# Kernel optimization log

Measured on AMD Instinct MI355X. Metric: run time of the kernel, lower is better.

The kernel has to match this reference:

```python
import jax, jax.numpy as jnp
import numpy as np

N, E, G = 20000, 320000, 64
IN_DIM, EDGE_DIM, H, L = 23, 6, 256, 4
NEG = 0.2   # leaky_relu negative slope (GATv2 default)
EPS = 1e-5  # layernorm eps


def setup_inputs() -> dict:
    key = jax.random.key(0)
    ks = jax.random.split(key, 12)
    g = lambda k, shape: jax.random.normal(k, shape, jnp.float32) * 0.05
    return {
        "x": jax.random.normal(ks[0], (N, IN_DIM), jnp.float32),
        "edge_index": jax.random.randint(ks[1], (2, E), 0, N),
        "edge_attr": jax.random.uniform(ks[2], (E, EDGE_DIM), dtype=jnp.float32),
        "batch": jnp.sort(jax.random.randint(ks[3], (N,), 0, G)),
        "W_l0": g(ks[4], (IN_DIM, H)),
        "W_r0": g(ks[5], (IN_DIM, H)),
        "W_l": g(ks[6], (L - 1, H, H)),
        "W_r": g(ks[7], (L - 1, H, H)),
        "b_l": jnp.zeros((L, H), jnp.float32),
        "b_r": jnp.zeros((L, H), jnp.float32),
        "W_e": g(ks[8], (L, EDGE_DIM, H)),
        "att": g(ks[9], (L, H)),
        "bias": jnp.zeros((L, H), jnp.float32),
        "ln_w": jnp.ones((L, H), jnp.float32),
        "ln_b": jnp.zeros((L, H), jnp.float32),
        "lin_W": g(ks[10], (H, H)),
        "lin_b": jnp.zeros((H,), jnp.float32),
    }


def _segment_softmax(logits, seg, n):
    m = jax.ops.segment_max(logits, seg, num_segments=n)  # every node has a self loop -> finite
    e = jnp.exp(logits - m[seg])
    s = jax.ops.segment_sum(e, seg, num_segments=n)
    return e / s[seg]


def _gatv2(h, src, dst, e_emb, Wl, bl, Wr, br, a, bout):
    n = h.shape[0]
    hl = h @ Wl + bl  # source transform [N, H]
    hr = h @ Wr + br  # target transform [N, H]
    m = hl[src] + hr[dst] + e_emb              # [E', H]
    m = jnp.where(m > 0, m, NEG * m)           # leaky_relu
    alpha = _segment_softmax(m @ a, dst, n)    # [E']
    out = jax.ops.segment_sum(hl[src] * alpha[:, None], dst, num_segments=n)
    return out + bout


def _layernorm(x, w, b):
    mu = x.mean(-1, keepdims=True)
    var = ((x - mu) ** 2).mean(-1, keepdims=True)
    return (x - mu) * jax.lax.rsqrt(var + EPS) * w + b


def reference(x, edge_index, edge_attr, batch, W_l0, W_r0, W_l, W_r, b_l, b_r,
              W_e, att, bias, ln_w, ln_b, lin_W, lin_b):
    n = x.shape[0]
    src, dst = edge_index[0], edge_index[1]
    # add self loops; self-loop edge_attr = mean of incoming edge_attr (fill_value='mean')
    ones_e = jnp.ones((src.shape[0],), x.dtype)
    deg = jax.ops.segment_sum(ones_e, dst, num_segments=n)
    loop_attr = jax.ops.segment_sum(edge_attr, dst, num_segments=n) / jnp.maximum(deg, 1.0)[:, None]
    loops = jnp.arange(n, dtype=src.dtype)
    src_f = jnp.concatenate([src, loops])
    dst_f = jnp.concatenate([dst, loops])
    ea = jnp.concatenate([edge_attr, loop_attr], axis=0)  # [E+N, 6]

    Wls = [W_l0] + [W_l[i] for i in range(L - 1)]
    Wrs = [W_r0] + [W_r[i] for i in range(L - 1)]
    h = x
    for i in range(L):
        e_emb = ea @ W_e[i]  # [E+N, H]
        h = _gatv2(h, src_f, dst_f, e_emb, Wls[i], b_l[i], Wrs[i], b_r[i], att[i], bias[i])
        h = _layernorm(h, ln_w[i], ln_b[i])
        h = jax.nn.relu(h)
    h = h @ lin_W + lin_b  # final jk='last' projection
    # global mean pool over graphs
    cnt = jax.ops.segment_sum(jnp.ones((n,), h.dtype), batch, num_segments=G)
    pooled = jax.ops.segment_sum(h, batch, num_segments=G) / jnp.maximum(cnt, 1.0)[:, None]
    return pooled
```

## Files before the change

### kernel.cpp

```cpp
#include <hip/hip_runtime.h>
#include <hip/hip_bf16.h>
#include <math.h>

#define H 256
#define EDIM 6
#define NEG 0.2f
#define LN_EPS 1e-5f
#define NPAD 20096

typedef __bf16 bf16x8 __attribute__((ext_vector_type(8)));
typedef float  floatx4 __attribute__((ext_vector_type(4)));
typedef float  f32x2   __attribute__((ext_vector_type(2)));

__device__ __forceinline__ float b2f(unsigned short u) {
    union { unsigned int i; float f; } v; v.i = ((unsigned int)u) << 16; return v.f;
}
__device__ __forceinline__ unsigned short f2bu(float f) {
    __hip_bfloat16 h = __float2bfloat16(f);
    return *(unsigned short*)&h;
}

__global__ void k_edge_hist(const int* __restrict__ ei, int* __restrict__ deg, int E) {
    int e = blockIdx.x * blockDim.x + threadIdx.x;
    if (e >= E) return;
    atomicAdd(&deg[ei[E + e]], 1);
}

__global__ __launch_bounds__(256) void k_scan1(const int* __restrict__ deg,
                                               int* __restrict__ row_ptr,
                                               int* __restrict__ bsum, int N) {
    __shared__ int ws[4];
    int tid = threadIdx.x, gid = blockIdx.x * 256 + tid;
    int lane = tid & 63, w = tid >> 6;
    int v = (gid < N) ? deg[gid] : 0;
    int x = v;
#pragma unroll
    for (int d = 1; d < 64; d <<= 1) { int y = __shfl_up(x, d); if (lane >= d) x += y; }
    if (lane == 63) ws[w] = x;
    __syncthreads();
    int off = 0;
#pragma unroll
    for (int i = 0; i < 4; i++) off += (i < w) ? ws[i] : 0;
    if (gid < N) row_ptr[gid] = off + x - v;
    if (tid == 255) bsum[blockIdx.x] = off + x;
}

__global__ __launch_bounds__(256) void k_scan2(int* __restrict__ bsum, int nb) {
    __shared__ int ws[4];
    int tid = threadIdx.x;
    int lane = tid & 63, w = tid >> 6;
    int v = (tid < nb) ? bsum[tid] : 0;
    int x = v;
#pragma unroll
    for (int d = 1; d < 64; d <<= 1) { int y = __shfl_up(x, d); if (lane >= d) x += y; }
    if (lane == 63) ws[w] = x;
    __syncthreads();
    int off = 0;
#pragma unroll
    for (int i = 0; i < 4; i++) off += (i < w) ? ws[i] : 0;
    if (tid < nb) bsum[tid] = off + x - v;
}

__global__ __launch_bounds__(256) void k_scan3(int* __restrict__ row_ptr,
                                               int* __restrict__ cursor,
                                               const int* __restrict__ bsum, int N, int E) {
    int gid = blockIdx.x * 256 + threadIdx.x;
    if (gid < N) {
        int v = row_ptr[gid] + bsum[blockIdx.x];
        row_ptr[gid] = v;
        cursor[gid] = v;
    }
    if (gid == 0) row_ptr[N] = E;
}

__global__ void k_scatter(const int* __restrict__ ei, const float* __restrict__ eattr,
                          int* __restrict__ cursor, float4* __restrict__ erec, int E) {
    int e = blockIdx.x * blockDim.x + threadIdx.x;
    if (e >= E) return;
    int s = ei[e], d = ei[E + e];
    int pos = atomicAdd(&cursor[d], 1);
    float4 ra, rb;
    ra.x = __int_as_float(s << 10);
    ra.y = eattr[e * EDIM + 0];
    ra.z = eattr[e * EDIM + 1];
    ra.w = eattr[e * EDIM + 2];
    rb.x = eattr[e * EDIM + 3];
    rb.y = eattr[e * EDIM + 4];
    rb.z = eattr[e * EDIM + 5];
    rb.w = 0.f;
    erec[(size_t)pos * 2]     = ra;
    erec[(size_t)pos * 2 + 1] = rb;
}

__global__ __launch_bounds__(256) void k_loop_mean(const int* __restrict__ row_ptr,
                                                   const float4* __restrict__ erec,
                                                   float* __restrict__ loop_attr, int N) {
    int wv = threadIdx.x >> 6, lane = threadIdx.x & 63;
    int node = blockIdx.x * 4 + wv;
    if (node >= N) return;
    int e0 = row_ptr[node], e1 = row_ptr[node + 1];
    float es[6] = {0.f, 0.f, 0.f, 0.f, 0.f, 0.f};
    for (int e = e0 + lane; e < e1; e += 64) {
        float4 ra = erec[(size_t)e * 2];
        float4 rb = erec[(size_t)e * 2 + 1];
        es[0] += ra.y; es[1] += ra.z; es[2] += ra.w;
        es[3] += rb.x; es[4] += rb.y; es[5] += rb.z;
    }
#pragma unroll
    for (int d = 1; d < 64; d <<= 1) {
#pragma unroll
        for (int k = 0; k < 6; k++) es[k] += __shfl_xor(es[k], d);
    }
    if (lane == 0) {
        float inv = 1.f / fmaxf((float)(e1 - e0), 1.f);
        float4 a, b;
        a.x = es[0] * inv; a.y = es[1] * inv; a.z = es[2] * inv; a.w = es[3] * inv;
        b.x = es[4] * inv; b.y = es[5] * inv; b.z = 0.f; b.w = 0.f;
        *(float4*)&loop_attr[(size_t)node * 8]     = a;
        *(float4*)&loop_attr[(size_t)node * 8 + 4] = b;
    }
}

__global__ __launch_bounds__(256) void k_conv_all(
    const float* __restrict__ x, const float* __restrict__ Wl0,
    const float* __restrict__ Wr0, const float* __restrict__ Wl,
    const float* __restrict__ Wr,
    __hip_bfloat16* __restrict__ xb, __hip_bfloat16* __restrict__ w0t,
    __hip_bfloat16* __restrict__ wbig, int N) {
    int idx = blockIdx.x * 256 + threadIdx.x;
    const int XN = NPAD * 32;
    if (idx < XN) {
        int r = idx >> 5, k = idx & 31;
        float v = (r < N && k < 23) ? x[r * 23 + k] : 0.f;
        xb[idx] = __float2bfloat16(v);
        return;
    }
    idx -= XN;
    if (idx < 16384) {
        int mat = idx >> 13, rem = idx & 8191;
        int c = rem >> 5, k = rem & 31;
        const float* W = mat ? Wr0 : Wl0;
        float v = (k < 23) ? W[k * 256 + c] : 0.f;
        w0t[idx] = __float2bfloat16(v);
        return;
    }
    idx -= 16384;
    if (idx < 6 * 65536) {
        int mat = idx >> 16, rem = idx & 65535;
        int c = rem >> 8, k = rem & 255;
        const float* W = (mat < 3) ? (Wl + (size_t)mat * 65536)
                       : (Wr + (size_t)(mat - 3) * 65536);
        wbig[idx] = __float2bfloat16(W[k * 256 + c]);
    }
}

template<int K>
__global__ __launch_bounds__(256) void k_gemm_mfma(
    const __hip_bfloat16* __restrict__ A, int N,
    const __hip_bfloat16* __restrict__ Wt1, const float* __restrict__ b1,
    float* __restrict__ C1,
    const __hip_bfloat16* __restrict__ Wt2, const float* __restrict__ b2,
    float* __restrict__ C2) {
    int tid = threadIdx.x;
    int wv = tid >> 6, lane = tid & 63;
    int quad = lane >> 4, l16 = lane & 15;
    int mat = blockIdx.x >> 1;
    int c0 = (blockIdx.x & 1) * 128;
    int r0 = blockIdx.y * 128;
    const __hip_bfloat16* Wt = mat ? Wt2 : Wt1;
    const float* bv = mat ? b2 : b1;
    float* C = mat ? C2 : C1;
    int wm = wv >> 1, wn = wv & 1;
    int rbase = r0 + wm * 64;
    int cbase = c0 + wn * 64;

    floatx4 acc[4][4] = {};
    const __bf16* Ab = (const __bf16*)A;
    const __bf16* Bb = (const __bf16*)Wt;

    if constexpr (K == 32) {
        bf16x8 a[4], b[4];
        const __bf16* Ap = Ab + (size_t)(rbase + l16) * K + quad * 8;
#pragma unroll
        for (int mi = 0; mi < 4; mi++)
            a[mi] = *(const bf16x8*)(Ap + (size_t)mi * 16 * K);
        const __bf16* Bp = Bb + (size_t)(cbase + l16) * K + quad * 8;
#pragma unroll
        for (int ni = 0; ni < 4; ni++)
            b[ni] = *(const bf16x8*)(Bp + (size_t)ni * 16 * K);
#pragma unroll
        for (int mi = 0; mi < 4; mi++)
#pragma unroll
            for (int ni = 0; ni < 4; ni++)
                acc[mi][ni] = __builtin_amdgcn_mfma_f32_16x16x32_bf16(a[mi], b[ni], acc[mi][ni], 0, 0, 0);
    } else {
        __shared__ __align__(16) __bf16 As[128 * 32];
        __shared__ __align__(16) __bf16 Bs[128 * 32];
        int srow = wv * 16 + (lane >> 2);
        int sseg = lane & 3;
        for (int k0 = 0; k0 < K; k0 += 32) {
#pragma unroll
            for (int j = 0; j < 2; j++) {
                int row = j * 64 + srow;
                const __bf16* gA = Ab + (size_t)(r0 + row) * K + k0 + sseg * 8;
                __builtin_amdgcn_global_load_lds(
                    (const __attribute__((address_space(1))) void*)gA,
                    (__attribute__((address_space(3))) void*)(As + j * 2048 + wv * 512),
                    16, 0, 0);
                const __bf16* gB = Bb + (size_t)(c0 + row) * K + k0 + sseg * 8;
                __builtin_amdgcn_global_load_lds(
                    (const __attribute__((address_space(1))) void*)gB,
                    (__attribute__((address_space(3))) void*)(Bs + j * 2048 + wv * 512),
                    16, 0, 0);
            }
            __syncthreads();
            bf16x8 a[4], b[4];
#pragma unroll
            for (int mi = 0; mi < 4; mi++)
                a[mi] = *(const bf16x8*)(As + (wm * 64 + mi * 16 + l16) * 32 + quad * 8);
#pragma unroll
            for (int ni = 0; ni < 4; ni++)
                b[ni] = *(const bf16x8*)(Bs + (wn * 64 + ni * 16 + l16) * 32 + quad * 8);
#pragma unroll
            for (int mi = 0; mi < 4; mi++)
#pragma unroll
                for (int ni = 0; ni < 4; ni++)
                    acc[mi][ni] = __builtin_amdgcn_mfma_f32_16x16x32_bf16(a[mi], b[ni], acc[mi][ni], 0, 0, 0);
            __syncthreads();
        }
    }
#pragma unroll
    for (int ni = 0; ni < 4; ni++) {
        int c = cbase + ni * 16 + l16;
        float bb = bv[c];
#pragma unroll
        for (int mi = 0; mi < 4; mi++) {
#pragma unroll
            for (int r = 0; r < 4; r++) {
                int gr = rbase + mi * 16 + quad * 4 + r;
                if (gr < N) C[(size_t)gr * H + c] = acc[mi][ni][r] + bb;
            }
        }
    }
}

__global__ __launch_bounds__(64) void k_gat(
    const float* __restrict__ hlf, const float* __restrict__ hr,
    const int* __restrict__ row_ptr, const float4* __restrict__ erec,
    const float* __restrict__ loop_attr,
    const float* __restrict__ We, const float* __restrict__ attv,
    const float* __restrict__ bias, const float* __restrict__ lnw,
    const float* __restrict__ lnb, unsigned short* __restrict__ hout, int N) {
    int lane = threadIdx.x & 63;
    int node = blockIdx.x;
    if (node >= N) return;
    int cb = lane * 4;
    int cb4 = cb * 4;
    const char* hbase = (const char*)hlf;
    bool b0 = (lane & 1) != 0;
    bool b1 = (lane & 2) != 0;

    f32x2 we2[EDIM][2];
#pragma unroll
    for (int k = 0; k < EDIM; k++) {
        float4 t = *(const float4*)&We[k * H + cb];
        we2[k][0] = (f32x2){t.x, t.y};
        we2[k][1] = (f32x2){t.z, t.w};
    }
    float4 t;
    t = *(const float4*)&attv[cb];
    f32x2 av0 = {t.x, t.y}, av1 = {t.z, t.w};
    t = *(const float4*)&hr[(size_t)node * H + cb];
    f32x2 hr0 = {t.x, t.y}, hr1 = {t.z, t.w};
    t = *(const float4*)&hlf[(size_t)node * H + cb];
    f32x2 hl0 = {t.x, t.y}, hl1 = {t.z, t.w};

    float denom = 0.f;
    f32x2 acc0 = {0.f, 0.f}, acc1 = {0.f, 0.f};

    int e0 = row_ptr[node], e1 = row_ptr[node + 1];
    int deg = e1 - e0;
    int gfull = deg >> 2;

    for (int g = 0; g <= gfull; g++) {
        int trem = (g == gfull) ? (deg & 3) : 4;
        if (trem == 0) break;
        int base = e0 + g * 4;
        f32x2 hsa[4], hsb[4];
        float p[4];
#pragma unroll
        for (int i = 0; i < 4; i++) {
            int idx = (i < trem) ? (base + i) : base;
            float4 ra = erec[(size_t)idx * 2];
            float4 rb = erec[(size_t)idx * 2 + 1];
            float4 h4 = *(const float4*)(hbase + (__float_as_int(ra.x) + cb4));
            hsa[i] = (f32x2){h4.x, h4.y};
            hsb[i] = (f32x2){h4.z, h4.w};
            f32x2 t0 = hr0, t1 = hr1;
            t0 += ra.y * we2[0][0]; t1 += ra.y * we2[0][1];
            t0 += ra.z * we2[1][0]; t1 += ra.z * we2[1][1];
            t0 += ra.w * we2[2][0]; t1 += ra.w * we2[2][1];
            t0 += rb.x * we2[3][0]; t1 += rb.x * we2[3][1];
            t0 += rb.y * we2[4][0]; t1 += rb.y * we2[4][1];
            t0 += rb.z * we2[5][0]; t1 += rb.z * we2[5][1];
            f32x2 v0 = hsa[i] + t0;
            f32x2 v1 = hsb[i] + t1;
            v0 = __builtin_elementwise_max(v0, v0 * NEG);
            v1 = __builtin_elementwise_max(v1, v1 * NEG);
            f32x2 pd = v0 * av0;
            pd += v1 * av1;
            p[i] = pd.x + pd.y;
        }
        float a01 = b0 ? p[1] : p[0];
        float c01 = b0 ? p[0] : p[1];
        a01 += __shfl_xor(c01, 1);
        float a23 = b0 ? p[3] : p[2];
        float c23 = b0 ? p[2] : p[3];
        a23 += __shfl_xor(c23, 1);
        float u = b1 ? a23 : a01;
        float v = b1 ? a01 : a23;
        u += __shfl_xor(v, 2);
        u += __shfl_xor(u, 4);
        u += __shfl_xor(u, 8);
        u += __shfl_xor(u, 16);
        u += __shfl_xor(u, 32);
        float w = ((lane & 3) < trem) ? __expf(u) : 0.f;
        float wx1 = __shfl_xor(w, 1);
        float wx2 = __shfl_xor(w, 2);
        float wx3 = __shfl_xor(wx1, 2);
        denom += (w + wx1) + (wx2 + wx3);
        float x0 = b0 ? wx1 : w,   x1 = b0 ? w   : wx1;
        float x2 = b0 ? wx3 : wx2, x3 = b0 ? wx2 : wx3;
        float w0 = b1 ? x2 : x0, w1 = b1 ? x3 : x1;
        float w2 = b1 ? x0 : x2, w3 = b1 ? x1 : x3;
        acc0 += w0 * hsa[0]; acc1 += w0 * hsb[0];
        acc0 += w1 * hsa[1]; acc1 += w1 * hsb[1];
        acc0 += w2 * hsa[2]; acc1 += w2 * hsb[2];
        acc0 += w3 * hsa[3]; acc1 += w3 * hsb[3];
    }

    {
        float4 la0 = *(const float4*)&loop_attr[(size_t)node * 8];
        float4 la1 = *(const float4*)&loop_attr[(size_t)node * 8 + 4];
        f32x2 t0 = hl0 + hr0, t1 = hl1 + hr1;
        t0 += la0.x * we2[0][0]; t1 += la0.x * we2[0][1];
        t0 += la0.y * we2[1][0]; t1 += la0.y * we2[1][1];
        t0 += la0.z * we2[2][0]; t1 += la0.z * we2[2][1];
        t0 += la0.w * we2[3][0]; t1 += la0.w * we2[3][1];
        t0 += la1.x * we2[4][0]; t1 += la1.x * we2[4][1];
        t0 += la1.y * we2[5][0]; t1 += la1.y * we2[5][1];
        t0 = __builtin_elementwise_max(t0, t0 * NEG);
        t1 = __builtin_elementwise_max(t1, t1 * NEG);
        f32x2 pd = t0 * av0;
        pd += t1 * av1;
        float p = pd.x + pd.y;
#pragma unroll
        for (int d = 1; d < 64; d <<= 1) p += __shfl_xor(p, d);
        float w = __expf(p);
        denom += w;
        acc0 += w * hl0; acc1 += w * hl1;
    }

    float inv = 1.f / denom;
    t = *(const float4*)&bias[cb];
    float o0 = acc0.x * inv + t.x;
    float o1 = acc0.y * inv + t.y;
    float o2 = acc1.x * inv + t.z;
    float o3 = acc1.y * inv + t.w;

    float s = (o0 + o1) + (o2 + o3);
    float q = fmaf(o0, o0, fmaf(o1, o1, fmaf(o2, o2, o3 * o3)));
    float a = b0 ? q : s;
    float c = b0 ? s : q;
    a += __shfl_xor(c, 1);
    a += __shfl_xor(a, 2);
    a += __shfl_xor(a, 4);
    a += __shfl_xor(a, 8);
    a += __shfl_xor(a, 16);
    a += __shfl_xor(a, 32);
    float other = __shfl_xor(a, 1);
    float stot = b0 ? other : a;
    float qtot = b0 ? a : other;
    float mu = stot * (1.f / 256.f);
    float var = fmaf(-mu, mu, qtot * (1.f / 256.f));
    float rstd = rsqrtf(fmaxf(var, 0.f) + LN_EPS);

    float4 w4 = *(const float4*)&lnw[cb];
    float4 b4 = *(const float4*)&lnb[cb];
    ushort4 outv;
    outv.x = f2bu(fmaxf((o0 - mu) * rstd * w4.x + b4.x, 0.f));
    outv.y = f2bu(fmaxf((o1 - mu) * rstd * w4.y + b4.y, 0.f));
    outv.z = f2bu(fmaxf((o2 - mu) * rstd * w4.z + b4.z, 0.f));
    outv.w = f2bu(fmaxf((o3 - mu) * rstd * w4.w + b4.w, 0.f));
    *(ushort4*)&hout[(size_t)node * H + cb] = outv;
}

__global__ __launch_bounds__(256) void k_pool_sum(
    const unsigned short* __restrict__ hb, const int* __restrict__ batch,
    float* __restrict__ pooled, int N) {
    int c = threadIdx.x;
    int chunk = (N + gridDim.x - 1) / gridDim.x;
    int n0 = blockIdx.x * chunk;
    int n1 = min(n0 + chunk, N);
    if (n0 >= n1) return;
    float acc = 0.f;
    int cur = batch[n0];
    for (int n = n0; n < n1; n++) {
        int g = batch[n];
        if (g != cur) {
            atomicAdd(&pooled[cur * H + c], acc);
            acc = 0.f; cur = g;
        }
        acc += b2f(hb[(size_t)n * H + c]);
    }
    atomicAdd(&pooled[cur * H + c], acc);
}

__global__ __launch_bounds__(256) void k_lin_pool(
    const float* __restrict__ pooled, const int* __restrict__ batch,
    const float* __restrict__ linW, const float* __restrict__ linb,
    float* __restrict__ out, int N) {
    __shared__ float row[H];
    __shared__ int s_lo, s_hi;
    int g = blockIdx.x, c = threadIdx.x;
    if (c == 0) {
        int lo = 0, hi = N;
        while (lo < hi) { int mid = (lo + hi) >> 1; if (batch[mid] < g) lo = mid + 1; else hi = mid; }
        s_lo = lo;
    }
    if (c == 1) {
        int lo = 0, hi = N;
        while (lo < hi) { int mid = (lo + hi) >> 1; if (batch[mid] < g + 1) lo = mid + 1; else hi = mid; }
        s_hi = lo;
    }
    __syncthreads();
    int cnt = s_hi - s_lo;
    float scale = (cnt > 0) ? 1.f / (float)cnt : 0.f;
    row[c] = pooled[g * H + c] * scale;
    __syncthreads();
    float acc = (cnt > 0) ? linb[c] : 0.f;
#pragma unroll 8
    for (int k = 0; k < H; k++) acc = fmaf(row[k], linW[k * H + c], acc);
    out[g * H + c] = acc;
}

extern "C" void kernel_launch(void* const* d_in, const int* in_sizes, int n_in,
                              void* d_out, int out_size, void* d_ws, size_t ws_size,
                              hipStream_t stream) {
    const float* x        = (const float*)d_in[0];
    const int*   ei       = (const int*)d_in[1];
    const float* eattr    = (const float*)d_in[2];
    const int*   batch    = (const int*)d_in[3];
    const float* W_l0     = (const float*)d_in[4];
    const float* W_r0     = (const float*)d_in[5];
    const float* W_l      = (const float*)d_in[6];
    const float* W_r      = (const float*)d_in[7];
    const float* b_l      = (const float*)d_in[8];
    const float* b_r      = (const float*)d_in[9];
    const float* W_e      = (const float*)d_in[10];
    const float* att      = (const float*)d_in[11];
    const float* bias     = (const float*)d_in[12];
    const float* ln_w     = (const float*)d_in[13];
    const float* ln_b     = (const float*)d_in[14];
    const float* lin_W    = (const float*)d_in[15];
    const float* lin_b    = (const float*)d_in[16];

    const int N = in_sizes[0] / 23;
    const int E = in_sizes[1] / 2;
    const int G = out_size / H;
    const int L = 4;

    char* p = (char*)d_ws;
    float* hlf = (float*)p;                       p += (size_t)N * H * 4;
    float* hr  = (float*)p;                       p += (size_t)N * H * 4;
    float4* erec = (float4*)p;                    p += (size_t)E * 32;
    unsigned short* hb = (unsigned short*)p;      p += (size_t)NPAD * H * 2;
    __hip_bfloat16* xb  = (__hip_bfloat16*)p;     p += (size_t)NPAD * 32 * 2;
    __hip_bfloat16* w0t = (__hip_bfloat16*)p;     p += (size_t)2 * 256 * 32 * 2;
    __hip_bfloat16* wbig = (__hip_bfloat16*)p;    p += (size_t)6 * 65536 * 2;
    float* loop_attr = (float*)p;                 p += (size_t)N * 8 * 4;
    float* pooled = (float*)p;                    p += (size_t)G * H * 4;
    int* deg      = (int*)p;                      p += (size_t)N * 4;
    int* row_ptr  = (int*)p;                      p += (size_t)(N + 1) * 4;
    int* cursor   = (int*)p;                      p += (size_t)N * 4;
    int* bsum     = (int*)p;                      p += (size_t)256 * 4;

    __hip_bfloat16* Wl0t = w0t;
    __hip_bfloat16* Wr0t = w0t + 8192;
    __hip_bfloat16* Wlt  = wbig;
    __hip_bfloat16* Wrt  = wbig + (size_t)3 * 65536;

    hipMemsetAsync(deg, 0, (size_t)N * sizeof(int), stream);
    hipMemsetAsync(pooled, 0, (size_t)G * H * sizeof(float), stream);
    hipMemsetAsync(hb + (size_t)N * H, 0, (size_t)(NPAD - N) * H * 2, stream);

    int tb = 256;
    int conv_total = NPAD * 32 + 16384 + 6 * 65536;
    k_conv_all<<<(conv_total + tb - 1) / tb, tb, 0, stream>>>(x, W_l0, W_r0, W_l, W_r,
                                                              xb, w0t, wbig, N);

    k_edge_hist<<<(E + tb - 1) / tb, tb, 0, stream>>>(ei, deg, E);
    int nb = (N + 255) / 256;
    k_scan1<<<nb, 256, 0, stream>>>(deg, row_ptr, bsum, N);
    k_scan2<<<1, 256, 0, stream>>>(bsum, nb);
    k_scan3<<<nb, 256, 0, stream>>>(row_ptr, cursor, bsum, N, E);
    k_scatter<<<(E + tb - 1) / tb, tb, 0, stream>>>(ei, eattr, cursor, erec, E);
    k_loop_mean<<<(N + 3) / 4, 256, 0, stream>>>(row_ptr, erec, loop_attr, N);

    dim3 gdual(4, NPAD / 128), blk(256);

    for (int l = 0; l < L; l++) {
        const __hip_bfloat16* A  = (l == 0) ? xb : (const __hip_bfloat16*)hb;
        const __hip_bfloat16* Wl = (l == 0) ? Wl0t : (Wlt + (size_t)(l - 1) * 65536);
        const __hip_bfloat16* Wr = (l == 0) ? Wr0t : (Wrt + (size_t)(l - 1) * 65536);
        if (l == 0)
            k_gemm_mfma<32><<<gdual, blk, 0, stream>>>(A, N, Wl, b_l + l * H, hlf,
                                                       Wr, b_r + l * H, hr);
        else
            k_gemm_mfma<256><<<gdual, blk, 0, stream>>>(A, N, Wl, b_l + l * H, hlf,
                                                        Wr, b_r + l * H, hr);
        k_gat<<<N, 64, 0, stream>>>(hlf, hr, row_ptr, erec, loop_attr,
                                    W_e + (size_t)l * EDIM * H, att + l * H,
                                    bias + l * H, ln_w + l * H, ln_b + l * H, hb, N);
    }

    k_pool_sum<<<256, 256, 0, stream>>>(hb, batch, pooled, N);
    k_lin_pool<<<G, 256, 0, stream>>>(pooled, batch, lin_W, lin_b, (float*)d_out, N);
}
```

Measured before the change: 460.0 us.

## Preload full weight slice into LDS once and fold memsets into conversion kernel

The K=256 GEMM path now loads the block's whole 128x256 weight slice into padded shared memory once, then reads A fragments directly from global memory each k-step. This drops the per-k-step LDS staging of both A and B and the two barriers per iteration. Separately, the three hipMemsetAsync calls are folded into the existing conversion kernel to cut launch overhead. In exchange, shared-memory use grows to about 66 KB per block, which may reduce occupancy, and A reads become uncoalesced strided global loads.

```diff
diff --git a/kernel.cpp b/kernel.cpp
--- a/kernel.cpp
+++ b/kernel.cpp
@@ -7,6 +7,7 @@
 #define NEG 0.2f
 #define LN_EPS 1e-5f
 #define NPAD 20096
+#define BSTRIDE 260
 
 typedef __bf16 bf16x8 __attribute__((ext_vector_type(8)));
 typedef float  floatx4 __attribute__((ext_vector_type(4)));
@@ -126,7 +127,8 @@
     const float* __restrict__ Wr0, const float* __restrict__ Wl,
     const float* __restrict__ Wr,
     __hip_bfloat16* __restrict__ xb, __hip_bfloat16* __restrict__ w0t,
-    __hip_bfloat16* __restrict__ wbig, int N) {
+    __hip_bfloat16* __restrict__ wbig, int* __restrict__ deg,
+    float* __restrict__ pooled, unsigned int* __restrict__ hbpad, int N) {
     int idx = blockIdx.x * 256 + threadIdx.x;
     const int XN = NPAD * 32;
     if (idx < XN) {
@@ -151,7 +153,14 @@
         const float* W = (mat < 3) ? (Wl + (size_t)mat * 65536)
                        : (Wr + (size_t)(mat - 3) * 65536);
         wbig[idx] = __float2bfloat16(W[k * 256 + c]);
-    }
+        return;
+    }
+    idx -= 6 * 65536;
+    if (idx < N) { deg[idx] = 0; return; }
+    idx -= N;
+    if (idx < 16384) { pooled[idx] = 0.f; return; }
+    idx -= 16384;
+    if (idx < (NPAD - 20000) * 128) hbpad[idx] = 0u;
 }
 
 template<int K>
@@ -194,39 +203,31 @@
             for (int ni = 0; ni < 4; ni++)
                 acc[mi][ni] = __builtin_amdgcn_mfma_f32_16x16x32_bf16(a[mi], b[ni], acc[mi][ni], 0, 0, 0);
     } else {
-        __shared__ __align__(16) __bf16 As[128 * 32];
-        __shared__ __align__(16) __bf16 Bs[128 * 32];
-        int srow = wv * 16 + (lane >> 2);
-        int sseg = lane & 3;
+        __shared__ __align__(16) __bf16 Bs[128 * BSTRIDE];
+#pragma unroll
+        for (int i = 0; i < 16; i++) {
+            int seg = tid + i * 256;
+            int col = seg >> 5;
+            int off = (seg & 31) * 8;
+            bf16x8 v = *(const bf16x8*)(Bb + (size_t)(c0 + col) * 256 + off);
+            *(bf16x8*)&Bs[col * BSTRIDE + off] = v;
+        }
+        __syncthreads();
+#pragma unroll 4
         for (int k0 = 0; k0 < K; k0 += 32) {
-#pragma unroll
-            for (int j = 0; j < 2; j++) {
-                int row = j * 64 + srow;
-                const __bf16* gA = Ab + (size_t)(r0 + row) * K + k0 + sseg * 8;
-                __builtin_amdgcn_global_load_lds(
-                    (const __attribute__((address_space(1))) void*)gA,
-                    (__attribute__((address_space(3))) void*)(As + j * 2048 + wv * 512),
-                    16, 0, 0);
-                const __bf16* gB = Bb + (size_t)(c0 + row) * K + k0 + sseg * 8;
-                __builtin_amdgcn_global_load_lds(
-                    (const __attribute__((address_space(1))) void*)gB,
-                    (__attribute__((address_space(3))) void*)(Bs + j * 2048 + wv * 512),
-                    16, 0, 0);
-            }
-            __syncthreads();
             bf16x8 a[4], b[4];
+            const __bf16* Ap = Ab + (size_t)(rbase + l16) * K + k0 + quad * 8;
 #pragma unroll
             for (int mi = 0; mi < 4; mi++)
-                a[mi] = *(const bf16x8*)(As + (wm * 64 + mi * 16 + l16) * 32 + quad * 8);
+                a[mi] = *(const bf16x8*)(Ap + (size_t)mi * 16 * K);
 #pragma unroll
             for (int ni = 0; ni < 4; ni++)
-                b[ni] = *(const bf16x8*)(Bs + (wn * 64 + ni * 16 + l16) * 32 + quad * 8);
+                b[ni] = *(const bf16x8*)&Bs[(wn * 64 + ni * 16 + l16) * BSTRIDE + k0 + quad * 8];
 #pragma unroll
             for (int mi = 0; mi < 4; mi++)
 #pragma unroll
                 for (int ni = 0; ni < 4; ni++)
                     acc[mi][ni] = __builtin_amdgcn_mfma_f32_16x16x32_bf16(a[mi], b[ni], acc[mi][ni], 0, 0, 0);
-            __syncthreads();
         }
     }
 #pragma unroll
@@ -490,14 +491,11 @@
     __hip_bfloat16* Wlt  = wbig;
     __hip_bfloat16* Wrt  = wbig + (size_t)3 * 65536;
 
-    hipMemsetAsync(deg, 0, (size_t)N * sizeof(int), stream);
-    hipMemsetAsync(pooled, 0, (size_t)G * H * sizeof(float), stream);
-    hipMemsetAsync(hb + (size_t)N * H, 0, (size_t)(NPAD - N) * H * 2, stream);
-
     int tb = 256;
-    int conv_total = NPAD * 32 + 16384 + 6 * 65536;
-    k_conv_all<<<(conv_total + tb - 1) / tb, tb, 0, stream>>>(x, W_l0, W_r0, W_l, W_r,
-                                                              xb, w0t, wbig, N);
+    int conv_total = NPAD * 32 + 16384 + 6 * 65536 + N + 16384 + (NPAD - N) * 128;
+    k_conv_all<<<(conv_total + tb - 1) / tb, tb, 0, stream>>>(
+        x, W_l0, W_r0, W_l, W_r, xb, w0t, wbig, deg, pooled,
+        (unsigned int*)(hb + (size_t)N * H), N);
 
     k_edge_hist<<<(E + tb - 1) / tb, tb, 0, stream>>>(ei, deg, E);
     int nb = (N + 255) / 256;
```

New measurement: 495.3 us. 7.7% more time.

## Store source-transform features in bf16 and fold memsets into conversion kernel

Applied to the files above, without the earlier changes.

The source-side transform hl is now written by the GEMM as bf16 instead of fp32, and the GAT kernel gathers it as ushort4 and widens it to float. This halves the bytes of the random per-edge gather and also halves the GEMM store traffic for that matrix. The stored source index shift moves from 10 to 9 to match the new row stride. Separately, the three hipMemsetAsync calls are folded into the existing conversion kernel to save launches. The cost is bf16 rounding of hl, which feeds both the attention logits and the aggregated messages.

```diff
diff --git a/kernel.cpp b/kernel.cpp
--- a/kernel.cpp
+++ b/kernel.cpp
@@ -80,7 +80,7 @@
     int s = ei[e], d = ei[E + e];
     int pos = atomicAdd(&cursor[d], 1);
     float4 ra, rb;
-    ra.x = __int_as_float(s << 10);
+    ra.x = __int_as_float(s << 9);
     ra.y = eattr[e * EDIM + 0];
     ra.z = eattr[e * EDIM + 1];
     ra.w = eattr[e * EDIM + 2];
@@ -126,7 +126,8 @@
     const float* __restrict__ Wr0, const float* __restrict__ Wl,
     const float* __restrict__ Wr,
     __hip_bfloat16* __restrict__ xb, __hip_bfloat16* __restrict__ w0t,
-    __hip_bfloat16* __restrict__ wbig, int N) {
+    __hip_bfloat16* __restrict__ wbig, int* __restrict__ deg,
+    float* __restrict__ pooled, unsigned int* __restrict__ hbpad, int N) {
     int idx = blockIdx.x * 256 + threadIdx.x;
     const int XN = NPAD * 32;
     if (idx < XN) {
@@ -151,14 +152,21 @@
         const float* W = (mat < 3) ? (Wl + (size_t)mat * 65536)
                        : (Wr + (size_t)(mat - 3) * 65536);
         wbig[idx] = __float2bfloat16(W[k * 256 + c]);
-    }
+        return;
+    }
+    idx -= 6 * 65536;
+    if (idx < N) { deg[idx] = 0; return; }
+    idx -= N;
+    if (idx < 16384) { pooled[idx] = 0.f; return; }
+    idx -= 16384;
+    if (idx < (NPAD - 20000) * 128) hbpad[idx] = 0u;
 }
 
 template<int K>
 __global__ __launch_bounds__(256) void k_gemm_mfma(
     const __hip_bfloat16* __restrict__ A, int N,
     const __hip_bfloat16* __restrict__ Wt1, const float* __restrict__ b1,
-    float* __restrict__ C1,
+    unsigned short* __restrict__ C1,
     const __hip_bfloat16* __restrict__ Wt2, const float* __restrict__ b2,
     float* __restrict__ C2) {
     int tid = threadIdx.x;
@@ -169,7 +177,6 @@
     int r0 = blockIdx.y * 128;
     const __hip_bfloat16* Wt = mat ? Wt2 : Wt1;
     const float* bv = mat ? b2 : b1;
-    float* C = mat ? C2 : C1;
     int wm = wv >> 1, wn = wv & 1;
     int rbase = r0 + wm * 64;
     int cbase = c0 + wn * 64;
@@ -238,14 +245,17 @@
 #pragma unroll
             for (int r = 0; r < 4; r++) {
                 int gr = rbase + mi * 16 + quad * 4 + r;
-                if (gr < N) C[(size_t)gr * H + c] = acc[mi][ni][r] + bb;
+                if (gr >= N) continue;
+                float val = acc[mi][ni][r] + bb;
+                if (mat == 0) C1[(size_t)gr * H + c] = f2bu(val);
+                else          C2[(size_t)gr * H + c] = val;
             }
         }
     }
 }
 
 __global__ __launch_bounds__(64) void k_gat(
-    const float* __restrict__ hlf, const float* __restrict__ hr,
+    const unsigned short* __restrict__ hlb, const float* __restrict__ hr,
     const int* __restrict__ row_ptr, const float4* __restrict__ erec,
     const float* __restrict__ loop_attr,
     const float* __restrict__ We, const float* __restrict__ attv,
@@ -255,8 +265,8 @@
     int node = blockIdx.x;
     if (node >= N) return;
     int cb = lane * 4;
-    int cb4 = cb * 4;
-    const char* hbase = (const char*)hlf;
+    int cb2 = lane * 8;
+    const char* hbase = (const char*)hlb;
     bool b0 = (lane & 1) != 0;
     bool b1 = (lane & 2) != 0;
 
@@ -272,8 +282,8 @@
     f32x2 av0 = {t.x, t.y}, av1 = {t.z, t.w};
     t = *(const float4*)&hr[(size_t)node * H + cb];
     f32x2 hr0 = {t.x, t.y}, hr1 = {t.z, t.w};
-    t = *(const float4*)&hlf[(size_t)node * H + cb];
-    f32x2 hl0 = {t.x, t.y}, hl1 = {t.z, t.w};
+    ushort4 hu = *(const ushort4*)&hlb[(size_t)node * H + cb];
+    f32x2 hl0 = {b2f(hu.x), b2f(hu.y)}, hl1 = {b2f(hu.z), b2f(hu.w)};
 
     float denom = 0.f;
     f32x2 acc0 = {0.f, 0.f}, acc1 = {0.f, 0.f};
@@ -293,9 +303,9 @@
             int idx = (i < trem) ? (base + i) : base;
             float4 ra = erec[(size_t)idx * 2];
             float4 rb = erec[(size_t)idx * 2 + 1];
-            float4 h4 = *(const float4*)(hbase + (__float_as_int(ra.x) + cb4));
-            hsa[i] = (f32x2){h4.x, h4.y};
-            hsb[i] = (f32x2){h4.z, h4.w};
+            ushort4 u4 = *(const ushort4*)(hbase + (__float_as_int(ra.x) + cb2));
+            hsa[i] = (f32x2){b2f(u4.x), b2f(u4.y)};
+            hsb[i] = (f32x2){b2f(u4.z), b2f(u4.w)};
             f32x2 t0 = hr0, t1 = hr1;
             t0 += ra.y * we2[0][0]; t1 += ra.y * we2[0][1];
             t0 += ra.z * we2[1][0]; t1 += ra.z * we2[1][1];
@@ -471,7 +481,7 @@
     const int L = 4;
 
     char* p = (char*)d_ws;
-    float* hlf = (float*)p;                       p += (size_t)N * H * 4;
+    unsigned short* hlb = (unsigned short*)p;     p += (size_t)N * H * 2;
     float* hr  = (float*)p;                       p += (size_t)N * H * 4;
     float4* erec = (float4*)p;                    p += (size_t)E * 32;
     unsigned short* hb = (unsigned short*)p;      p += (size_t)NPAD * H * 2;
@@ -490,14 +500,11 @@
     __hip_bfloat16* Wlt  = wbig;
     __hip_bfloat16* Wrt  = wbig + (size_t)3 * 65536;
 
-    hipMemsetAsync(deg, 0, (size_t)N * sizeof(int), stream);
-    hipMemsetAsync(pooled, 0, (size_t)G * H * sizeof(float), stream);
-    hipMemsetAsync(hb + (size_t)N * H, 0, (size_t)(NPAD - N) * H * 2, stream);
-
     int tb = 256;
-    int conv_total = NPAD * 32 + 16384 + 6 * 65536;
-    k_conv_all<<<(conv_total + tb - 1) / tb, tb, 0, stream>>>(x, W_l0, W_r0, W_l, W_r,
-                                                              xb, w0t, wbig, N);
+    int conv_total = NPAD * 32 + 16384 + 6 * 65536 + N + 16384 + (NPAD - N) * 128;
+    k_conv_all<<<(conv_total + tb - 1) / tb, tb, 0, stream>>>(
+        x, W_l0, W_r0, W_l, W_r, xb, w0t, wbig, deg, pooled,
+        (unsigned int*)(hb + (size_t)N * H), N);
 
     k_edge_hist<<<(E + tb - 1) / tb, tb, 0, stream>>>(ei, deg, E);
     int nb = (N + 255) / 256;
@@ -514,12 +521,12 @@
         const __hip_bfloat16* Wl = (l == 0) ? Wl0t : (Wlt + (size_t)(l - 1) * 65536);
         const __hip_bfloat16* Wr = (l == 0) ? Wr0t : (Wrt + (size_t)(l - 1) * 65536);
         if (l == 0)
-            k_gemm_mfma<32><<<gdual, blk, 0, stream>>>(A, N, Wl, b_l + l * H, hlf,
+            k_gemm_mfma<32><<<gdual, blk, 0, stream>>>(A, N, Wl, b_l + l * H, hlb,
                                                        Wr, b_r + l * H, hr);
         else
-            k_gemm_mfma<256><<<gdual, blk, 0, stream>>>(A, N, Wl, b_l + l * H, hlf,
+            k_gemm_mfma<256><<<gdual, blk, 0, stream>>>(A, N, Wl, b_l + l * H, hlb,
                                                         Wr, b_r + l * H, hr);
-        k_gat<<<N, 64, 0, stream>>>(hlf, hr, row_ptr, erec, loop_attr,
+        k_gat<<<N, 64, 0, stream>>>(hlb, hr, row_ptr, erec, loop_attr,
                                     W_e + (size_t)l * EDIM * H, att + l * H,
                                     bias + l * H, ln_w + l * H, ln_b + l * H, hb, N);
     }
```

Result: faster. 430.0 us (-6.5%).
